# Performance work log

Measured on AMD Instinct MI355X. Metric: run time of the kernel, lower is better.

## Reference

```python
import jax, jax.numpy as jnp
import numpy as np

NUM_CHANNELS = 512
B_DIM = 64
C_DIM = 16
N = 512
FEAT = NUM_CHANNELS * 4 * 4  # 8192


def setup_inputs() -> dict:
    key = jax.random.key(0)
    k1, k2 = jax.random.split(key)
    inp = jax.random.normal(k1, (N, NUM_CHANNELS, 4, 4), dtype=jnp.float32)
    T = jax.random.normal(k2, (FEAT, B_DIM * C_DIM), dtype=jnp.float32) * 0.1
    return {"inp": inp, "T": T}


def reference(inp, T):
    x = inp.reshape(-1, FEAT)                      # (N, 8192)
    M = (x @ T).reshape(-1, B_DIM, C_DIM)          # (N, B, C)
    # pairwise L1 distance over C: (N, N, B)
    dist = jnp.sum(jnp.abs(M[:, None, :, :] - M[None, :, :, :]), axis=-1)
    o = jnp.sum(jnp.exp(-dist), axis=1)            # (N, B)
    return jnp.concatenate((x, o), axis=1)         # (N, 8192 + B)
```

## Files before the change

kernel.cpp:

```cpp
#include <hip/hip_runtime.h>

#define NROWS 512
#define FEAT  8192
#define BDIM  64
#define CDIM  16
#define MCOLS 1024
#define OUTC  8256
#define KSPLIT 8
#define KCHUNK (FEAT / KSPLIT)
#define KSTEPS (KCHUNK / 64)
#define MSIZE  (NROWS * MCOLS)

typedef __bf16 bf16x8 __attribute__((ext_vector_type(8)));
typedef float  floatx4 __attribute__((ext_vector_type(4)));

static __device__ __forceinline__ unsigned int pk2(float a, float b) {
    unsigned short lo = __builtin_bit_cast(unsigned short, (__bf16)a);
    unsigned short hi = __builtin_bit_cast(unsigned short, (__bf16)b);
    return (unsigned int)lo | ((unsigned int)hi << 16);
}

__global__ __launch_bounds__(512, 2) void k_gemm(const float* __restrict__ x,
                                                 const float* __restrict__ T,
                                                 float* __restrict__ Mp) {
    __shared__ __align__(16) unsigned short ldsA[128 * 64];
    __shared__ __align__(16) unsigned short ldsB[128 * 64];
    char* ldsAc = (char*)ldsA;
    char* ldsBc = (char*)ldsB;

    int bid = blockIdx.x;
    int wg = (bid & 7) * 32 + (bid >> 3);
    int mt = wg & 3, nt = (wg >> 2) & 7, ks = wg >> 5;
    int m0 = mt * 128, n0 = nt * 128, kbase = ks * KCHUNK;
    int t = threadIdx.x, w = t >> 6, l = t & 63;

    int arow = t >> 4, aq = t & 15;
    const float* gA = x + (size_t)(m0 + arow) * FEAT + kbase + aq * 4;
    int swa = (arow & 7) ^ ((arow >> 2) & 7);
    int wA = arow * 128 + (((aq >> 1) ^ swa) << 4) + ((aq & 1) << 3);

    int n4 = t & 31, kg = t >> 5;
    const float* gB = T + (size_t)(kbase + kg * 4) * MCOLS + n0 + n4 * 4;
    int wB[4];
#pragma unroll
    for (int j = 0; j < 4; ++j) {
        int n = n4 * 4 + j;
        int swn = (n & 7) ^ ((n >> 2) & 7);
        wB[j] = n * 128 + (((kg >> 1) ^ swn) << 4) + ((kg & 1) << 3);
    }

    int wr = w >> 2, wc = w & 3, fm = l & 15, fq = l >> 4;
    int swf = (fm & 7) ^ ((fm >> 2) & 7);
    int baseA = (wr * 64 + fm) * 128 + ((fq ^ swf) << 4);
    int baseB = (wc * 32 + fm) * 128 + ((fq ^ swf) << 4);

    float4 va[4], vb[4];
    auto issue = [&](int KK) {
        int kko = KK * 64;
        va[0] = *(const float4*)(gA + kko);
        va[1] = *(const float4*)(gA + 32 * FEAT + kko);
        va[2] = *(const float4*)(gA + 64 * FEAT + kko);
        va[3] = *(const float4*)(gA + 96 * FEAT + kko);
        vb[0] = *(const float4*)(gB + (size_t)(kko + 0) * MCOLS);
        vb[1] = *(const float4*)(gB + (size_t)(kko + 1) * MCOLS);
        vb[2] = *(const float4*)(gB + (size_t)(kko + 2) * MCOLS);
        vb[3] = *(const float4*)(gB + (size_t)(kko + 3) * MCOLS);
    };

    issue(0);
    floatx4 acc[4][2] = {};

    for (int kk = 0; kk < KSTEPS; ++kk) {
#pragma unroll
        for (int r = 0; r < 4; ++r) {
            uint2 u; u.x = pk2(va[r].x, va[r].y); u.y = pk2(va[r].z, va[r].w);
            *(uint2*)(ldsAc + wA + r * 4096) = u;
        }
        {
            uint2 u;
            u.x = pk2(vb[0].x, vb[1].x); u.y = pk2(vb[2].x, vb[3].x);
            *(uint2*)(ldsBc + wB[0]) = u;
            u.x = pk2(vb[0].y, vb[1].y); u.y = pk2(vb[2].y, vb[3].y);
            *(uint2*)(ldsBc + wB[1]) = u;
            u.x = pk2(vb[0].z, vb[1].z); u.y = pk2(vb[2].z, vb[3].z);
            *(uint2*)(ldsBc + wB[2]) = u;
            u.x = pk2(vb[0].w, vb[1].w); u.y = pk2(vb[2].w, vb[3].w);
            *(uint2*)(ldsBc + wB[3]) = u;
        }
        __syncthreads();
        if (kk + 1 < KSTEPS) issue(kk + 1);
#pragma unroll
        for (int h = 0; h < 2; ++h) {
            bf16x8 af[4], bfr[2];
#pragma unroll
            for (int a = 0; a < 4; ++a)
                af[a] = *(const bf16x8*)(ldsAc + ((baseA + a * 2048) ^ ((h ^ (a & 1)) << 6)));
#pragma unroll
            for (int b = 0; b < 2; ++b)
                bfr[b] = *(const bf16x8*)(ldsBc + ((baseB + b * 2048) ^ ((h ^ (b & 1)) << 6)));
#pragma unroll
            for (int a = 0; a < 4; ++a)
#pragma unroll
                for (int b = 0; b < 2; ++b)
                    acc[a][b] = __builtin_amdgcn_mfma_f32_16x16x32_bf16(af[a], bfr[b], acc[a][b], 0, 0, 0);
        }
        __syncthreads();
    }

    float* outp = Mp + (size_t)ks * MSIZE;
    int gr0 = m0 + wr * 64, gc0 = n0 + wc * 32;
#pragma unroll
    for (int a = 0; a < 4; ++a)
#pragma unroll
        for (int r = 0; r < 4; ++r) {
            int row = gr0 + a * 16 + fq * 4 + r;
#pragma unroll
            for (int b = 0; b < 2; ++b)
                outp[(size_t)row * MCOLS + gc0 + b * 16 + fm] = acc[a][b][r];
        }
}

__global__ __launch_bounds__(512, 2) void k_pair(const float* __restrict__ x,
                                                 const float* __restrict__ Mp,
                                                 float* __restrict__ out) {
    __shared__ float ldsM[NROWS * 20];
    __shared__ float partial[8][64];
    int bid = blockIdx.x, t = threadIdx.x;
    int b = bid & 63, itp = bid >> 6;

    float4 cv[8];
    {
        const float* src = x + (size_t)bid * 2 * FEAT;
#pragma unroll
        for (int i = 0; i < 8; ++i) {
            int idx = t + i * 512;
            cv[i] = *(const float4*)(src + (size_t)(idx >> 11) * FEAT + (idx & 2047) * 4);
        }
    }

#pragma unroll
    for (int p = 0; p < 4; ++p) {
        int idx = t + p * 512;
        int j = idx >> 2, c4 = idx & 3;
        const float* base = Mp + (size_t)j * MCOLS + b * CDIM + c4 * 4;
        float4 s = *(const float4*)base;
#pragma unroll
        for (int k = 1; k < KSPLIT; ++k) {
            float4 v = *(const float4*)(base + (size_t)k * MSIZE);
            s.x += v.x; s.y += v.y; s.z += v.z; s.w += v.w;
        }
        *(float4*)&ldsM[j * 20 + c4 * 4] = s;
    }
    __syncthreads();

    int lane = t & 63, w = t >> 6, g = t >> 8, wg = (t >> 6) & 3;
    int i = (itp * 2 + g) * 64 + lane;
    float mi[CDIM];
#pragma unroll
    for (int cc = 0; cc < CDIM; ++cc) mi[cc] = ldsM[i * 20 + cc];

    float acc = 0.0f;
    for (int jj = wg * 128; jj < wg * 128 + 128; ++jj) {
        float d = 0.0f;
#pragma unroll
        for (int cc = 0; cc < CDIM; ++cc) d += fabsf(mi[cc] - ldsM[jj * 20 + cc]);
        acc += __expf(-d);
    }
    partial[w][lane] = acc;
    __syncthreads();
    if ((t & 255) < 64) {
        int ii = (itp * 2 + g) * 64 + (t & 63);
        float o = partial[g * 4 + 0][t & 63] + partial[g * 4 + 1][t & 63] +
                  partial[g * 4 + 2][t & 63] + partial[g * 4 + 3][t & 63];
        out[(size_t)ii * OUTC + FEAT + b] = o;
    }

    {
        float* dst = out + (size_t)bid * 2 * OUTC;
#pragma unroll
        for (int i2 = 0; i2 < 8; ++i2) {
            int idx = t + i2 * 512;
            *(float4*)(dst + (size_t)(idx >> 11) * OUTC + (idx & 2047) * 4) = cv[i2];
        }
    }
}

extern "C" void kernel_launch(void* const* d_in, const int* in_sizes, int n_in,
                              void* d_out, int out_size, void* d_ws, size_t ws_size,
                              hipStream_t stream) {
    const float* x = (const float*)d_in[0];
    const float* T = (const float*)d_in[1];
    float* out = (float*)d_out;

    float* Mp = (float*)d_ws;

    k_gemm<<<256, 512, 0, stream>>>(x, T, Mp);
    k_pair<<<256, 512, 0, stream>>>(x, Mp, out);
}
```

Baseline: 145.3 us.

## Double-buffer GEMM LDS tiles with two-deep prefetch; move x copy earlier in pair kernel

The GEMM kernel now keeps two LDS buffers and two register staging sets. Global loads are issued two k-steps ahead, which leaves one barrier per step instead of two. This is meant to hide global load latency and cut synchronisation, at the cost of more LDS (64KB per block) and more registers, which may reduce occupancy. The pair kernel also copies x into the output right after the partial-sum reduction, so the 8 float4 values no longer stay live in registers through the pairwise loop.

```diff
diff --git a/kernel.cpp b/kernel.cpp
--- a/kernel.cpp
+++ b/kernel.cpp
@@ -23,8 +23,8 @@
 __global__ __launch_bounds__(512, 2) void k_gemm(const float* __restrict__ x,
                                                  const float* __restrict__ T,
                                                  float* __restrict__ Mp) {
-    __shared__ __align__(16) unsigned short ldsA[128 * 64];
-    __shared__ __align__(16) unsigned short ldsB[128 * 64];
+    __shared__ __align__(16) unsigned short ldsA[2][128 * 64];
+    __shared__ __align__(16) unsigned short ldsB[2][128 * 64];
     char* ldsAc = (char*)ldsA;
     char* ldsBc = (char*)ldsB;
 
@@ -54,57 +54,64 @@
     int baseA = (wr * 64 + fm) * 128 + ((fq ^ swf) << 4);
     int baseB = (wc * 32 + fm) * 128 + ((fq ^ swf) << 4);
 
-    float4 va[4], vb[4];
-    auto issue = [&](int KK) {
-        int kko = KK * 64;
-        va[0] = *(const float4*)(gA + kko);
-        va[1] = *(const float4*)(gA + 32 * FEAT + kko);
-        va[2] = *(const float4*)(gA + 64 * FEAT + kko);
-        va[3] = *(const float4*)(gA + 96 * FEAT + kko);
-        vb[0] = *(const float4*)(gB + (size_t)(kko + 0) * MCOLS);
-        vb[1] = *(const float4*)(gB + (size_t)(kko + 1) * MCOLS);
-        vb[2] = *(const float4*)(gB + (size_t)(kko + 2) * MCOLS);
-        vb[3] = *(const float4*)(gB + (size_t)(kko + 3) * MCOLS);
+    floatx4 acc[4][2] = {};
+    float4 va0[4], vb0[4], va1[4], vb1[4];
+
+    auto issue = [&](int KK, float4* A4, float4* B4) {
+        const float* pa = gA + KK * 64;
+        A4[0] = *(const float4*)(pa);
+        A4[1] = *(const float4*)(pa + 32 * FEAT);
+        A4[2] = *(const float4*)(pa + 64 * FEAT);
+        A4[3] = *(const float4*)(pa + 96 * FEAT);
+        const float* pb = gB + (size_t)KK * 64 * MCOLS;
+        B4[0] = *(const float4*)(pb);
+        B4[1] = *(const float4*)(pb + MCOLS);
+        B4[2] = *(const float4*)(pb + 2 * MCOLS);
+        B4[3] = *(const float4*)(pb + 3 * MCOLS);
     };
 
-    issue(0);
-    floatx4 acc[4][2] = {};
-
-    for (int kk = 0; kk < KSTEPS; ++kk) {
+    auto step = [&](int KK, int SO, float4* A4, float4* B4) {
 #pragma unroll
         for (int r = 0; r < 4; ++r) {
-            uint2 u; u.x = pk2(va[r].x, va[r].y); u.y = pk2(va[r].z, va[r].w);
-            *(uint2*)(ldsAc + wA + r * 4096) = u;
+            uint2 u; u.x = pk2(A4[r].x, A4[r].y); u.y = pk2(A4[r].z, A4[r].w);
+            *(uint2*)(ldsAc + SO + wA + r * 4096) = u;
         }
         {
             uint2 u;
-            u.x = pk2(vb[0].x, vb[1].x); u.y = pk2(vb[2].x, vb[3].x);
-            *(uint2*)(ldsBc + wB[0]) = u;
-            u.x = pk2(vb[0].y, vb[1].y); u.y = pk2(vb[2].y, vb[3].y);
-            *(uint2*)(ldsBc + wB[1]) = u;
-            u.x = pk2(vb[0].z, vb[1].z); u.y = pk2(vb[2].z, vb[3].z);
-            *(uint2*)(ldsBc + wB[2]) = u;
-            u.x = pk2(vb[0].w, vb[1].w); u.y = pk2(vb[2].w, vb[3].w);
-            *(uint2*)(ldsBc + wB[3]) = u;
+            u.x = pk2(B4[0].x, B4[1].x); u.y = pk2(B4[2].x, B4[3].x);
+            *(uint2*)(ldsBc + SO + wB[0]) = u;
+            u.x = pk2(B4[0].y, B4[1].y); u.y = pk2(B4[2].y, B4[3].y);
+            *(uint2*)(ldsBc + SO + wB[1]) = u;
+            u.x = pk2(B4[0].z, B4[1].z); u.y = pk2(B4[2].z, B4[3].z);
+            *(uint2*)(ldsBc + SO + wB[2]) = u;
+            u.x = pk2(B4[0].w, B4[1].w); u.y = pk2(B4[2].w, B4[3].w);
+            *(uint2*)(ldsBc + SO + wB[3]) = u;
         }
-        __syncthreads();
-        if (kk + 1 < KSTEPS) issue(kk + 1);
+        if (KK + 2 < KSTEPS) issue(KK + 2, A4, B4);
+        asm volatile("s_waitcnt lgkmcnt(0)" ::: "memory");
+        __builtin_amdgcn_s_barrier();
 #pragma unroll
         for (int h = 0; h < 2; ++h) {
             bf16x8 af[4], bfr[2];
 #pragma unroll
             for (int a = 0; a < 4; ++a)
-                af[a] = *(const bf16x8*)(ldsAc + ((baseA + a * 2048) ^ ((h ^ (a & 1)) << 6)));
+                af[a] = *(const bf16x8*)(ldsAc + SO + ((baseA + a * 2048) ^ ((h ^ (a & 1)) << 6)));
 #pragma unroll
             for (int b = 0; b < 2; ++b)
-                bfr[b] = *(const bf16x8*)(ldsBc + ((baseB + b * 2048) ^ ((h ^ (b & 1)) << 6)));
+                bfr[b] = *(const bf16x8*)(ldsBc + SO + ((baseB + b * 2048) ^ ((h ^ (b & 1)) << 6)));
 #pragma unroll
             for (int a = 0; a < 4; ++a)
 #pragma unroll
                 for (int b = 0; b < 2; ++b)
                     acc[a][b] = __builtin_amdgcn_mfma_f32_16x16x32_bf16(af[a], bfr[b], acc[a][b], 0, 0, 0);
         }
-        __syncthreads();
+    };
+
+    issue(0, va0, vb0);
+    issue(1, va1, vb1);
+    for (int kk = 0; kk < KSTEPS; kk += 2) {
+        step(kk,     0,     va0, vb0);
+        step(kk + 1, 16384, va1, vb1);
     }
 
     float* outp = Mp + (size_t)ks * MSIZE;
@@ -128,16 +135,6 @@
     int bid = blockIdx.x, t = threadIdx.x;
     int b = bid & 63, itp = bid >> 6;
 
-    float4 cv[8];
-    {
-        const float* src = x + (size_t)bid * 2 * FEAT;
-#pragma unroll
-        for (int i = 0; i < 8; ++i) {
-            int idx = t + i * 512;
-            cv[i] = *(const float4*)(src + (size_t)(idx >> 11) * FEAT + (idx & 2047) * 4);
-        }
-    }
-
 #pragma unroll
     for (int p = 0; p < 4; ++p) {
         int idx = t + p * 512;
@@ -150,6 +147,17 @@
             s.x += v.x; s.y += v.y; s.z += v.z; s.w += v.w;
         }
         *(float4*)&ldsM[j * 20 + c4 * 4] = s;
+    }
+
+    {
+        const float* src = x + (size_t)bid * 2 * FEAT;
+        float* dst = out + (size_t)bid * 2 * OUTC;
+#pragma unroll
+        for (int i = 0; i < 8; ++i) {
+            int idx = t + i * 512;
+            float4 v = *(const float4*)(src + (size_t)(idx >> 11) * FEAT + (idx & 2047) * 4);
+            *(float4*)(dst + (size_t)(idx >> 11) * OUTC + (idx & 2047) * 4) = v;
+        }
     }
     __syncthreads();
 
@@ -174,15 +182,6 @@
                   partial[g * 4 + 2][t & 63] + partial[g * 4 + 3][t & 63];
         out[(size_t)ii * OUTC + FEAT + b] = o;
     }
-
-    {
-        float* dst = out + (size_t)bid * 2 * OUTC;
-#pragma unroll
-        for (int i2 = 0; i2 < 8; ++i2) {
-            int idx = t + i2 * 512;
-            *(float4*)(dst + (size_t)(idx >> 11) * OUTC + (idx & 2047) * 4) = cv[i2];
-        }
-    }
 }
 
 extern "C" void kernel_launch(void* const* d_in, const int* in_sizes, int n_in,
```

Measured after the change: 130.3 us. 1.11x faster.
